# Optimization experiments

Hardware: AMD Instinct MI355X
Metric: run time of the kernel (lower is better)

Reference implementation:

```python
import jax, jax.numpy as jnp
import numpy as np

N_NODES = 100000
N_EDGES = 1600000
HID = 64
EPS = 1e-5


def setup_inputs() -> dict:
    key = jax.random.key(0)
    ks = jax.random.split(key, 16)
    d = {}
    d["x"] = jax.random.normal(ks[0], (N_NODES, 3), dtype=jnp.float32)
    d["edge_index"] = jax.random.randint(ks[1], (2, N_EDGES), 0, N_NODES, dtype=jnp.int64)
    # GCNConv weights (glorot-ish scaling)
    d["W1"] = jax.random.normal(ks[2], (3, HID), dtype=jnp.float32) * 0.3
    d["b1"] = jnp.zeros((HID,), jnp.float32)
    d["W2"] = jax.random.normal(ks[3], (HID, HID), dtype=jnp.float32) * (1.0 / np.sqrt(HID))
    d["b2"] = jnp.zeros((HID,), jnp.float32)
    d["W3"] = jax.random.normal(ks[4], (HID, HID), dtype=jnp.float32) * (1.0 / np.sqrt(HID))
    d["b3"] = jnp.zeros((HID,), jnp.float32)
    # edge predictor MLP: 128 -> 64 -> 32 -> 2 with BatchNorm after first two ReLUs
    d["Wm1"] = jax.random.normal(ks[5], (2 * HID, HID), dtype=jnp.float32) * (1.0 / np.sqrt(2 * HID))
    d["bm1"] = jnp.zeros((HID,), jnp.float32)
    d["g1"] = jnp.ones((HID,), jnp.float32)
    d["be1"] = jnp.zeros((HID,), jnp.float32)
    d["Wm2"] = jax.random.normal(ks[6], (HID, HID // 2), dtype=jnp.float32) * (1.0 / np.sqrt(HID))
    d["bm2"] = jnp.zeros((HID // 2,), jnp.float32)
    d["g2"] = jnp.ones((HID // 2,), jnp.float32)
    d["be2"] = jnp.zeros((HID // 2,), jnp.float32)
    d["Wm3"] = jax.random.normal(ks[7], (HID // 2, 2), dtype=jnp.float32) * (1.0 / np.sqrt(HID // 2))
    d["bm3"] = jnp.zeros((2,), jnp.float32)
    return d


def _gcn_conv(h_in, W, b, row, col, n_nodes):
    """PyG GCNConv: y = D^{-1/2}(A+I)D^{-1/2} (x W) + b (self-loops in row/col)."""
    h = h_in @ W  # [N, out]
    deg = jax.ops.segment_sum(jnp.ones_like(col, dtype=h.dtype), col, num_segments=n_nodes)
    dinv = jnp.where(deg > 0, jax.lax.rsqrt(deg), 0.0)
    norm = dinv[row] * dinv[col]  # [E+N]
    msg = h[row] * norm[:, None]  # gather + per-edge scale
    out = jax.ops.segment_sum(msg, col, num_segments=n_nodes)
    return out + b


def _batchnorm(x, gamma, beta):
    # training-mode batch statistics (biased variance), eps as in nn.BatchNorm1d
    mu = jnp.mean(x, axis=0)
    var = jnp.mean(jnp.square(x - mu), axis=0)
    return (x - mu) * jax.lax.rsqrt(var + EPS) * gamma + beta


def reference(x, edge_index, W1, b1, W2, b2, W3, b3,
              Wm1, bm1, g1, be1, Wm2, bm2, g2, be2, Wm3, bm3):
    n = x.shape[0]
    loops = jnp.arange(n, dtype=edge_index.dtype)
    row = jnp.concatenate([edge_index[0], loops])
    col = jnp.concatenate([edge_index[1], loops])

    h = jax.nn.relu(_gcn_conv(x, W1, b1, row, col, n))
    h = jax.nn.relu(_gcn_conv(h, W2, b2, row, col, n))
    h = _gcn_conv(h, W3, b3, row, col, n)

    src, dst = edge_index[0], edge_index[1]
    ef = jnp.concatenate([h[src], h[dst]], axis=1)  # [E, 2*HID]

    z = jax.nn.relu(ef @ Wm1 + bm1)
    z = _batchnorm(z, g1, be1)
    z = jax.nn.relu(z @ Wm2 + bm2)
    z = _batchnorm(z, g2, be2)
    return z @ Wm3 + bm3  # [E, 2]
```

## Files before the change

### kernel.cpp

```cpp
#include <hip/hip_runtime.h>
#include <hip/hip_bf16.h>
#include <cstdint>
#include <cstring>

#define NN 100000
#define NE 1600000
#define HID 64
#define EPS 1e-5f

typedef __bf16 bf16_t;
typedef __attribute__((ext_vector_type(8))) __bf16 bf16x8;
typedef __attribute__((ext_vector_type(4))) float f32x4;
typedef __attribute__((ext_vector_type(2))) float f32x2;
typedef __attribute__((ext_vector_type(16))) float f32x16;

#define LDS_FENCE() asm volatile("s_waitcnt lgkmcnt(0)" ::: "memory")

__global__ void k_detect(const unsigned* __restrict__ xw, const int* __restrict__ eiw,
                         int* __restrict__ flags) {
  int lane = threadIdx.x;
  unsigned u = xw[lane];
  unsigned lo = u & 0xFFFFu;
  unsigned e = (lo >> 7) & 0xFFu;
  bool bf_ok = (lo == 0u) || (e >= 0x50u && e <= 0x8Fu);
  unsigned long long b1 = __ballot(bf_ok);
  int v = eiw[2 * lane + 1];
  unsigned long long b2 = __ballot(v == 0);
  if (lane == 0) {
    flags[0] = (b1 == ~0ull) ? 1 : 0;
    flags[1] = (b2 == ~0ull) ? 1 : 0;
  }
}

struct FPtrs {
  const void* p[17];
  int len[17];
  int ofs[17];
};

template <typename FT>
__global__ void k_cvt_f(FPtrs fp, float* __restrict__ canon, const int* __restrict__ flags,
                        int total) {
  if (flags[0] != (int)(sizeof(FT) == 2)) return;
  int i = blockIdx.x * blockDim.x + threadIdx.x;
  int stride = gridDim.x * blockDim.x;
  for (int t = i; t < total; t += stride) {
    int seg = 0;
    while (seg < 16 && t >= fp.ofs[seg] + fp.len[seg]) ++seg;
    canon[t] = (float)((const FT*)fp.p[seg])[t - fp.ofs[seg]];
  }
}

template <typename IT>
__global__ void k_cvt_idx(const IT* __restrict__ ei, int* __restrict__ eic,
                          const int* __restrict__ flags) {
  if (flags[1] != (int)(sizeof(IT) == 8)) return;
  int i = blockIdx.x * blockDim.x + threadIdx.x;
  int stride = gridDim.x * blockDim.x;
  for (int t = i; t < 2 * NE; t += stride) eic[t] = (int)ei[t];
}

__global__ void k_zero4(f32x4* __restrict__ p, int n4) {
  int i = blockIdx.x * blockDim.x + threadIdx.x;
  int stride = gridDim.x * blockDim.x;
  f32x4 z = {0.f, 0.f, 0.f, 0.f};
  for (int t = i; t < n4; t += stride) p[t] = z;
}

__global__ void k_count(const int* __restrict__ col, int* __restrict__ cnt) {
  int i = blockIdx.x * blockDim.x + threadIdx.x;
  int stride = gridDim.x * blockDim.x;
  for (int e = i; e < NE; e += stride) atomicAdd(&cnt[col[e]], 1);
}

__global__ void k_dinv(const int* __restrict__ cnt, float* __restrict__ d) {
  int n = blockIdx.x * blockDim.x + threadIdx.x;
  if (n < NN) d[n] = rsqrtf((float)cnt[n] + 1.0f);
}

__global__ void k_scan1(const int* __restrict__ cnt, int* __restrict__ rowptr,
                        int* __restrict__ bsum, int nvals) {
  __shared__ int tmp[256];
  int gid = blockIdx.x * 256 + threadIdx.x;
  int v = (gid < nvals) ? cnt[gid] : 0;
  tmp[threadIdx.x] = v;
  __syncthreads();
  for (int s = 1; s < 256; s <<= 1) {
    int add = (threadIdx.x >= s) ? tmp[threadIdx.x - s] : 0;
    __syncthreads();
    tmp[threadIdx.x] += add;
    __syncthreads();
  }
  if (gid < nvals) rowptr[gid] = tmp[threadIdx.x] - v;
  if (threadIdx.x == 255) bsum[blockIdx.x] = tmp[255];
}

__global__ void k_scan2(int* __restrict__ bsum, int* __restrict__ btop, int nblocks) {
  __shared__ int tmp[512];
  int v = (threadIdx.x < nblocks) ? bsum[threadIdx.x] : 0;
  tmp[threadIdx.x] = v;
  __syncthreads();
  for (int s = 1; s < 512; s <<= 1) {
    int add = (threadIdx.x >= s) ? tmp[threadIdx.x - s] : 0;
    __syncthreads();
    tmp[threadIdx.x] += add;
    __syncthreads();
  }
  if (threadIdx.x < nblocks) btop[threadIdx.x] = tmp[threadIdx.x] - v;
}

__global__ void k_scan3(int* __restrict__ rowptr, const int* __restrict__ btop,
                        int* __restrict__ cursor, int nvals) {
  int gid = blockIdx.x * 256 + threadIdx.x;
  if (gid < nvals) {
    int v = rowptr[gid] + btop[blockIdx.x];
    rowptr[gid] = v;
    cursor[gid] = v;
  }
}

__global__ void k_fill(const int* __restrict__ eic, int* __restrict__ cursor,
                       int* __restrict__ csr_src) {
  int i = blockIdx.x * blockDim.x + threadIdx.x;
  int stride = gridDim.x * blockDim.x;
  for (int e = i; e < NE; e += stride) {
    int src = eic[e], dst = eic[NE + e];
    int pos = atomicAdd(&cursor[dst], 1);
    csr_src[pos] = src;
  }
}

__global__ void k_xs(const float* __restrict__ x, const float* __restrict__ dinv,
                     f32x4* __restrict__ xs4) {
  int n = blockIdx.x * blockDim.x + threadIdx.x;
  if (n >= NN) return;
  float d = dinv[n];
  f32x4 r = {x[n * 3 + 0] * d, x[n * 3 + 1] * d, x[n * 3 + 2] * d, 0.f};
  xs4[n] = r;
}

__global__ __launch_bounds__(256) void k_g1(const int* __restrict__ rowptr,
                                            const int* __restrict__ cnt,
                                            const int* __restrict__ csr_src,
                                            const f32x4* __restrict__ xs4,
                                            const float* __restrict__ dinv,
                                            f32x4* __restrict__ agg3) {
  int wid = (blockIdx.x * blockDim.x + threadIdx.x) >> 6;
  int nw = (gridDim.x * blockDim.x) >> 6;
  int lane = threadIdx.x & 63;
  int comp = lane & 3, slot = lane >> 2;
  for (int n = wid; n < NN; n += nw) {
    int beg = rowptr[n], c = cnt[n];
    float acc = 0.f;
    for (int k = slot; k < c; k += 16) {
      int src = csr_src[beg + k];
      acc += ((const float*)(xs4 + src))[comp];
    }
    acc += __shfl_xor(acc, 4); acc += __shfl_xor(acc, 8);
    acc += __shfl_xor(acc, 16); acc += __shfl_xor(acc, 32);
    if (lane < 4) {
      float self = ((const float*)(xs4 + n))[comp];
      ((float*)(agg3 + n))[comp] = (acc + self) * dinv[n];
    }
  }
}

__global__ __launch_bounds__(512) void k_f1(const f32x4* __restrict__ agg3,
                                            const float* __restrict__ W1f,
                                            const float* __restrict__ b1f,
                                            const float* __restrict__ W2f,
                                            const float* __restrict__ dinv,
                                            float* __restrict__ hs) {
  __shared__ float W1l[192];
  __shared__ float b1l[64];
  __shared__ float W2l[64 * 64];
  __shared__ float hrow[8][64];
  int tid = threadIdx.x;
  if (tid < 192) W1l[tid] = W1f[tid];
  if (tid < 64) b1l[tid] = b1f[tid];
  for (int i = tid; i < 64 * 64; i += 512) W2l[i] = W2f[i];
  __syncthreads();
  int w = tid >> 6, j = tid & 63;
  for (int nb = blockIdx.x * 8 + w; nb < NN; nb += gridDim.x * 8) {
    f32x4 a = agg3[nb];
    float h = fmaxf(a[0] * W1l[j] + a[1] * W1l[64 + j] + a[2] * W1l[128 + j] + b1l[j], 0.f);
    hrow[w][j] = h;
    LDS_FENCE();
    float acc = 0.f;
#pragma unroll 8
    for (int k = 0; k < 64; ++k) acc += hrow[w][k] * W2l[k * 64 + j];
    hs[nb * 64 + j] = acc * dinv[nb];
  }
}

__global__ __launch_bounds__(512) void k_g2(const int* __restrict__ rowptr,
                                            const int* __restrict__ cnt,
                                            const int* __restrict__ csr_src,
                                            const float* __restrict__ hs,
                                            const float* __restrict__ dinv,
                                            const float* __restrict__ b2f,
                                            const float* __restrict__ W3f,
                                            float* __restrict__ hs3) {
  __shared__ float W3l[64 * 64];
  __shared__ float hrow[8][64];
  int tid = threadIdx.x;
  for (int i = tid; i < 64 * 64; i += 512) W3l[i] = W3f[i];
  __syncthreads();
  int w = tid >> 6, j = tid & 63;
  float rb = b2f[j];
  for (int n = blockIdx.x * 8 + w; n < NN; n += gridDim.x * 8) {
    int beg = rowptr[n], c = cnt[n];
    float acc = hs[n * 64 + j];
    int k = 0;
    for (; k + 8 <= c; k += 8) {
      int s0 = csr_src[beg + k + 0], s1 = csr_src[beg + k + 1];
      int s2 = csr_src[beg + k + 2], s3 = csr_src[beg + k + 3];
      int s4 = csr_src[beg + k + 4], s5 = csr_src[beg + k + 5];
      int s6 = csr_src[beg + k + 6], s7 = csr_src[beg + k + 7];
      float v0 = hs[s0 * 64 + j], v1 = hs[s1 * 64 + j];
      float v2 = hs[s2 * 64 + j], v3 = hs[s3 * 64 + j];
      float v4 = hs[s4 * 64 + j], v5 = hs[s5 * 64 + j];
      float v6 = hs[s6 * 64 + j], v7 = hs[s7 * 64 + j];
      acc += ((v0 + v1) + (v2 + v3)) + ((v4 + v5) + (v6 + v7));
    }
    for (; k < c; ++k) acc += hs[csr_src[beg + k] * 64 + j];
    float h2 = fmaxf(acc * dinv[n] + rb, 0.f);
    hrow[w][j] = h2;
    LDS_FENCE();
    float s = 0.f;
#pragma unroll 8
    for (int kk = 0; kk < 64; ++kk) s += hrow[w][kk] * W3l[kk * 64 + j];
    hs3[n * 64 + j] = s * dinv[n];
  }
}

__global__ __launch_bounds__(512) void k_g3(const int* __restrict__ rowptr,
                                            const int* __restrict__ cnt,
                                            const int* __restrict__ csr_src,
                                            const float* __restrict__ hs3,
                                            const float* __restrict__ dinv,
                                            const float* __restrict__ b3f,
                                            const float* __restrict__ Wm1f,
                                            bf16_t* __restrict__ u, bf16_t* __restrict__ v) {
  __shared__ float Wt[64 * 64];
  __shared__ float Wb[64 * 64];
  __shared__ float hrow[8][64];
  int tid = threadIdx.x;
  for (int i = tid; i < 64 * 64; i += 512) {
    Wt[i] = Wm1f[i];
    Wb[i] = Wm1f[4096 + i];
  }
  __syncthreads();
  int w = tid >> 6, j = tid & 63;
  float rb = b3f[j];
  for (int n = blockIdx.x * 8 + w; n < NN; n += gridDim.x * 8) {
    int beg = rowptr[n], c = cnt[n];
    float acc = hs3[n * 64 + j];
    int k = 0;
    for (; k + 8 <= c; k += 8) {
      int s0 = csr_src[beg + k + 0], s1 = csr_src[beg + k + 1];
      int s2 = csr_src[beg + k + 2], s3 = csr_src[beg + k + 3];
      int s4 = csr_src[beg + k + 4], s5 = csr_src[beg + k + 5];
      int s6 = csr_src[beg + k + 6], s7 = csr_src[beg + k + 7];
      float v0 = hs3[s0 * 64 + j], v1 = hs3[s1 * 64 + j];
      float v2 = hs3[s2 * 64 + j], v3 = hs3[s3 * 64 + j];
      float v4 = hs3[s4 * 64 + j], v5 = hs3[s5 * 64 + j];
      float v6 = hs3[s6 * 64 + j], v7 = hs3[s7 * 64 + j];
      acc += ((v0 + v1) + (v2 + v3)) + ((v4 + v5) + (v6 + v7));
    }
    for (; k < c; ++k) acc += hs3[csr_src[beg + k] * 64 + j];
    float h3 = acc * dinv[n] + rb;
    hrow[w][j] = h3;
    LDS_FENCE();
    float au = 0.f, av = 0.f;
#pragma unroll 8
    for (int kk = 0; kk < 64; ++kk) {
      float hv = hrow[w][kk];
      au += hv * Wt[kk * 64 + j];
      av += hv * Wb[kk * 64 + j];
    }
    u[n * 64 + j] = (bf16_t)au;
    v[n * 64 + j] = (bf16_t)av;
  }
}

__global__ __launch_bounds__(256) void k_e1(const int* __restrict__ eic,
                                            const bf16_t* __restrict__ u,
                                            const bf16_t* __restrict__ v,
                                            const float* __restrict__ bm1f,
                                            float* __restrict__ sum1,
                                            float* __restrict__ sq1) {
  __shared__ float reds[16][16];
  __shared__ float redq[16][16];
  int lane = threadIdx.x & 63;
  int wv = threadIdx.x >> 6;
  int wave = blockIdx.x * 4 + wv;
  int nwaves = gridDim.x * 4;
  int n = lane & 15, q = lane >> 4;
  f32x16 bk;
#pragma unroll
  for (int j = 0; j < 8; ++j) {
    bk[j] = bm1f[q * 8 + j];
    bk[8 + j] = bm1f[32 + q * 8 + j];
  }
  f32x16 accs = {};
  f32x16 accq = {};
#pragma unroll 2
  for (int t = wave; t < NE / 16; t += nwaves) {
    int e = t * 16 + n;
    int src = eic[e], dst = eic[NE + e];
    const bf16x8* pu = (const bf16x8*)(u + src * 64);
    const bf16x8* pv = (const bf16x8*)(v + dst * 64);
    bf16x8 ua = pu[q], ub = pu[4 + q], va = pv[q], vb = pv[4 + q];
    f32x16 a1k;
#pragma unroll
    for (int j = 0; j < 8; ++j) {
      a1k[j] = fmaxf((float)ua[j] + (float)va[j] + bk[j], 0.f);
      a1k[8 + j] = fmaxf((float)ub[j] + (float)vb[j] + bk[8 + j], 0.f);
    }
    accs += a1k;
    accq += a1k * a1k;
  }
#pragma unroll
  for (int j = 0; j < 16; ++j) {
    float s = accs[j], qq = accq[j];
    s += __shfl_xor(s, 1); s += __shfl_xor(s, 2);
    s += __shfl_xor(s, 4); s += __shfl_xor(s, 8);
    qq += __shfl_xor(qq, 1); qq += __shfl_xor(qq, 2);
    qq += __shfl_xor(qq, 4); qq += __shfl_xor(qq, 8);
    if (n == 0) {
      reds[wv * 4 + q][j] = s;
      redq[wv * 4 + q][j] = qq;
    }
  }
  __syncthreads();
  int tid = threadIdx.x;
  if (tid < 64) {
    int jq = (tid & 31) >> 3, elem = (tid >> 5) * 8 + (tid & 7);
    float s = reds[jq][elem] + reds[4 + jq][elem] + reds[8 + jq][elem] + reds[12 + jq][elem];
    float qq = redq[jq][elem] + redq[4 + jq][elem] + redq[8 + jq][elem] + redq[12 + jq][elem];
    unsafeAtomicAdd(&sum1[tid], s);
    unsafeAtomicAdd(&sq1[tid], qq);
  }
}

__global__ void k_bnconst(const float* __restrict__ sum, const float* __restrict__ sq,
                          const float* __restrict__ g, const float* __restrict__ be,
                          float* __restrict__ sarr, float* __restrict__ tarr, int ncol) {
  int j = threadIdx.x;
  if (j >= ncol) return;
  float mu = sum[j] / (float)NE;
  float var = fmaxf(sq[j] / (float)NE - mu * mu, 0.f);
  float s = g[j] * rsqrtf(var + EPS);
  sarr[j] = s;
  tarr[j] = be[j] - mu * s;
}

template <bool STORE>
__global__ __launch_bounds__(256) void k_e2(const int* __restrict__ eic,
                                            const bf16_t* __restrict__ u,
                                            const bf16_t* __restrict__ v,
                                            const float* __restrict__ bm1f,
                                            const float* __restrict__ s1, const float* __restrict__ t1,
                                            const float* __restrict__ Wm2f,
                                            const float* __restrict__ bm2f,
                                            bf16_t* __restrict__ a2s,
                                            float* __restrict__ sum2,
                                            float* __restrict__ sq2) {
  __shared__ float red2[4][4][16];
  int lane = threadIdx.x & 63;
  int wv = threadIdx.x >> 6;
  int wave = blockIdx.x * 4 + wv;
  int nwaves = gridDim.x * 4;
  int n = lane & 15, q = lane >> 4;
  f32x16 bk, s1k, t1k;
#pragma unroll
  for (int j = 0; j < 8; ++j) {
    bk[j] = bm1f[q * 8 + j];       bk[8 + j] = bm1f[32 + q * 8 + j];
    s1k[j] = s1[q * 8 + j];        s1k[8 + j] = s1[32 + q * 8 + j];
    t1k[j] = t1[q * 8 + j];        t1k[8 + j] = t1[32 + q * 8 + j];
  }
  bf16x8 b2h00, b2h01, b2h10, b2h11;
#pragma unroll
  for (int j = 0; j < 8; ++j) {
    b2h00[j] = (bf16_t)Wm2f[(q * 8 + j) * 32 + 0 * 16 + n];
    b2h01[j] = (bf16_t)Wm2f[(q * 8 + j) * 32 + 1 * 16 + n];
    b2h10[j] = (bf16_t)Wm2f[(32 + q * 8 + j) * 32 + 0 * 16 + n];
    b2h11[j] = (bf16_t)Wm2f[(32 + q * 8 + j) * 32 + 1 * 16 + n];
  }
  float bias20 = bm2f[n], bias21 = bm2f[16 + n];
  float accs0 = 0.f, accs1 = 0.f, accq0 = 0.f, accq1 = 0.f;
  for (int t = wave; t < NE / 16; t += nwaves) {
    int e = t * 16 + n;
    int src = eic[e], dst = eic[NE + e];
    const bf16x8* pu = (const bf16x8*)(u + src * 64);
    const bf16x8* pv = (const bf16x8*)(v + dst * 64);
    bf16x8 ua = pu[q], ub = pu[4 + q], va = pv[q], vb = pv[4 + q];
    f32x16 a1k;
#pragma unroll
    for (int j = 0; j < 8; ++j) {
      a1k[j] = fmaxf((float)ua[j] + (float)va[j] + bk[j], 0.f);
      a1k[8 + j] = fmaxf((float)ub[j] + (float)vb[j] + bk[8 + j], 0.f);
    }
    f32x16 z = a1k * s1k + t1k;
    bf16x8 g0h, g0l, g1h, g1l;
#pragma unroll
    for (int j = 0; j < 8; ++j) {
      float z0 = z[j], z1 = z[8 + j];
      bf16_t h0 = (bf16_t)z0, h1 = (bf16_t)z1;
      g0h[j] = h0; g0l[j] = (bf16_t)(z0 - (float)h0);
      g1h[j] = h1; g1l[j] = (bf16_t)(z1 - (float)h1);
    }
    f32x4 c0 = {0.f, 0.f, 0.f, 0.f}, c1 = {0.f, 0.f, 0.f, 0.f};
    c0 = __builtin_amdgcn_mfma_f32_16x16x32_bf16(g0h, b2h00, c0, 0, 0, 0);
    c0 = __builtin_amdgcn_mfma_f32_16x16x32_bf16(g0l, b2h00, c0, 0, 0, 0);
    c0 = __builtin_amdgcn_mfma_f32_16x16x32_bf16(g1h, b2h10, c0, 0, 0, 0);
    c0 = __builtin_amdgcn_mfma_f32_16x16x32_bf16(g1l, b2h10, c0, 0, 0, 0);
    c1 = __builtin_amdgcn_mfma_f32_16x16x32_bf16(g0h, b2h01, c1, 0, 0, 0);
    c1 = __builtin_amdgcn_mfma_f32_16x16x32_bf16(g0l, b2h01, c1, 0, 0, 0);
    c1 = __builtin_amdgcn_mfma_f32_16x16x32_bf16(g1h, b2h11, c1, 0, 0, 0);
    c1 = __builtin_amdgcn_mfma_f32_16x16x32_bf16(g1l, b2h11, c1, 0, 0, 0);
#pragma unroll
    for (int r = 0; r < 4; ++r) {
      float v0 = fmaxf(c0[r] + bias20, 0.f);
      float v1 = fmaxf(c1[r] + bias21, 0.f);
      if (STORE) {
        a2s[(size_t)(t * 16 + q * 4 + r) * 32 + n] = (bf16_t)v0;
        a2s[(size_t)(t * 16 + q * 4 + r) * 32 + 16 + n] = (bf16_t)v1;
      }
      accs0 += v0; accq0 += v0 * v0;
      accs1 += v1; accq1 += v1 * v1;
    }
  }
  accs0 += __shfl_xor(accs0, 16); accs0 += __shfl_xor(accs0, 32);
  accq0 += __shfl_xor(accq0, 16); accq0 += __shfl_xor(accq0, 32);
  accs1 += __shfl_xor(accs1, 16); accs1 += __shfl_xor(accs1, 32);
  accq1 += __shfl_xor(accq1, 16); accq1 += __shfl_xor(accq1, 32);
  if (lane < 16) {
    red2[wv][0][lane] = accs0;
    red2[wv][1][lane] = accq0;
    red2[wv][2][lane] = accs1;
    red2[wv][3][lane] = accq1;
  }
  __syncthreads();
  int tid = threadIdx.x;
  if (tid < 32) {
    int which = tid >> 4, nn = tid & 15;
    float s = red2[0][which * 2][nn] + red2[1][which * 2][nn] + red2[2][which * 2][nn] +
              red2[3][which * 2][nn];
    float qq = red2[0][which * 2 + 1][nn] + red2[1][which * 2 + 1][nn] +
               red2[2][which * 2 + 1][nn] + red2[3][which * 2 + 1][nn];
    unsafeAtomicAdd(&sum2[tid], s);
    unsafeAtomicAdd(&sq2[tid], qq);
  }
}

template <typename OT>
__global__ __launch_bounds__(256) void k_out_stream(const bf16_t* __restrict__ a2s,
                                                    const float* __restrict__ s2,
                                                    const float* __restrict__ t2,
                                                    const float* __restrict__ Wm3f,
                                                    const float* __restrict__ bm3f,
                                                    OT* __restrict__ out,
                                                    const int* __restrict__ flags) {
  if (flags[0] != (int)(sizeof(OT) == 2)) return;
  int lane = threadIdx.x & 63;
  int wave = blockIdx.x * 4 + (threadIdx.x >> 6);
  int nwaves = gridDim.x * 4;
  int half = lane & 1;
  int sub = lane >> 1;
  f32x16 s2c, t2c, w0, w1;
#pragma unroll
  for (int i = 0; i < 16; ++i) {
    int c = half * 16 + i;
    s2c[i] = s2[c]; t2c[i] = t2[c];
    w0[i] = Wm3f[c * 2 + 0]; w1[i] = Wm3f[c * 2 + 1];
  }
  float bb0 = bm3f[0], bb1 = bm3f[1];
  const int ntiles = NE / 32;
#pragma unroll 2
  for (int t = wave; t < ntiles; t += nwaves) {
    int e = t * 32 + sub;
    const bf16x8* pa = (const bf16x8*)(a2s + (size_t)e * 32 + half * 16);
    bf16x8 v0 = pa[0], v1 = pa[1];
    float o0 = 0.f, o1 = 0.f;
#pragma unroll
    for (int i = 0; i < 8; ++i) {
      float z = (float)v0[i] * s2c[i] + t2c[i];
      o0 += z * w0[i]; o1 += z * w1[i];
      float z2 = (float)v1[i] * s2c[8 + i] + t2c[8 + i];
      o0 += z2 * w0[8 + i]; o1 += z2 * w1[8 + i];
    }
    o0 += __shfl_xor(o0, 1);
    o1 += __shfl_xor(o1, 1);
    if (half == 0) {
      o0 += bb0; o1 += bb1;
      if (sizeof(OT) == 2) {
        bf16_t p[2] = {(bf16_t)o0, (bf16_t)o1};
        unsigned pw;
        memcpy(&pw, p, 4);
        ((unsigned*)out)[e] = pw;
      } else {
        f32x2 pw = {o0, o1};
        ((f32x2*)out)[e] = pw;
      }
    }
  }
}

template <typename OT>
__global__ __launch_bounds__(256) void k_out_recomp(const int* __restrict__ eic,
                                                    const bf16_t* __restrict__ u,
                                                    const bf16_t* __restrict__ v,
                                                    const float* __restrict__ bm1f,
                                                    const float* __restrict__ s1, const float* __restrict__ t1,
                                                    const float* __restrict__ Wm2f,
                                                    const float* __restrict__ bm2f,
                                                    const float* __restrict__ s2, const float* __restrict__ t2,
                                                    const float* __restrict__ Wm3f,
                                                    const float* __restrict__ bm3f,
                                                    OT* __restrict__ out,
                                                    const int* __restrict__ flags) {
  if (flags[0] != (int)(sizeof(OT) == 2)) return;
  int lane = threadIdx.x & 63;
  int wave = blockIdx.x * 4 + (threadIdx.x >> 6);
  int nwaves = gridDim.x * 4;
  int n = lane & 15, q = lane >> 4;
  f32x16 bk, s1k, t1k;
#pragma unroll
  for (int j = 0; j < 8; ++j) {
    bk[j] = bm1f[q * 8 + j];       bk[8 + j] = bm1f[32 + q * 8 + j];
    s1k[j] = s1[q * 8 + j];        s1k[8 + j] = s1[32 + q * 8 + j];
    t1k[j] = t1[q * 8 + j];        t1k[8 + j] = t1[32 + q * 8 + j];
  }
  bf16x8 b2h00, b2h01, b2h10, b2h11;
#pragma unroll
  for (int j = 0; j < 8; ++j) {
    b2h00[j] = (bf16_t)Wm2f[(q * 8 + j) * 32 + 0 * 16 + n];
    b2h01[j] = (bf16_t)Wm2f[(q * 8 + j) * 32 + 1 * 16 + n];
    b2h10[j] = (bf16_t)Wm2f[(32 + q * 8 + j) * 32 + 0 * 16 + n];
    b2h11[j] = (bf16_t)Wm2f[(32 + q * 8 + j) * 32 + 1 * 16 + n];
  }
  float bias20 = bm2f[n], bias21 = bm2f[16 + n];
  float s2c0 = s2[n], t2c0 = t2[n], s2c1 = s2[16 + n], t2c1 = t2[16 + n];
  float w3a0 = Wm3f[n * 2 + 0], w3a1 = Wm3f[n * 2 + 1];
  float w3b0 = Wm3f[(16 + n) * 2 + 0], w3b1 = Wm3f[(16 + n) * 2 + 1];
  float bb0 = bm3f[0], bb1 = bm3f[1];

  for (int t = wave; t < NE / 16; t += nwaves) {
    int e = t * 16 + n;
    int src = eic[e], dst = eic[NE + e];
    const bf16x8* pu = (const bf16x8*)(u + src * 64);
    const bf16x8* pv = (const bf16x8*)(v + dst * 64);
    bf16x8 ua = pu[q], ub = pu[4 + q], va = pv[q], vb = pv[4 + q];
    f32x16 a1k;
#pragma unroll
    for (int j = 0; j < 8; ++j) {
      a1k[j] = fmaxf((float)ua[j] + (float)va[j] + bk[j], 0.f);
      a1k[8 + j] = fmaxf((float)ub[j] + (float)vb[j] + bk[8 + j], 0.f);
    }
    f32x16 z = a1k * s1k + t1k;
    bf16x8 g0h, g0l, g1h, g1l;
#pragma unroll
    for (int j = 0; j < 8; ++j) {
      float z0 = z[j], z1 = z[8 + j];
      bf16_t h0 = (bf16_t)z0, h1 = (bf16_t)z1;
      g0h[j] = h0; g0l[j] = (bf16_t)(z0 - (float)h0);
      g1h[j] = h1; g1l[j] = (bf16_t)(z1 - (float)h1);
    }
    f32x4 c0 = {0.f, 0.f, 0.f, 0.f}, c1 = {0.f, 0.f, 0.f, 0.f};
    c0 = __builtin_amdgcn_mfma_f32_16x16x32_bf16(g0h, b2h00, c0, 0, 0, 0);
    c0 = __builtin_amdgcn_mfma_f32_16x16x32_bf16(g0l, b2h00, c0, 0, 0, 0);
    c0 = __builtin_amdgcn_mfma_f32_16x16x32_bf16(g1h, b2h10, c0, 0, 0, 0);
    c0 = __builtin_amdgcn_mfma_f32_16x16x32_bf16(g1l, b2h10, c0, 0, 0, 0);
    c1 = __builtin_amdgcn_mfma_f32_16x16x32_bf16(g0h, b2h01, c1, 0, 0, 0);
    c1 = __builtin_amdgcn_mfma_f32_16x16x32_bf16(g0l, b2h01, c1, 0, 0, 0);
    c1 = __builtin_amdgcn_mfma_f32_16x16x32_bf16(g1h, b2h11, c1, 0, 0, 0);
    c1 = __builtin_amdgcn_mfma_f32_16x16x32_bf16(g1l, b2h11, c1, 0, 0, 0);
#pragma unroll
    for (int r = 0; r < 4; ++r) {
      float z0 = fmaxf(c0[r] + bias20, 0.f) * s2c0 + t2c0;
      float z1 = fmaxf(c1[r] + bias21, 0.f) * s2c1 + t2c1;
      float o0 = z0 * w3a0 + z1 * w3b0;
      float o1 = z0 * w3a1 + z1 * w3b1;
      o0 += __shfl_xor(o0, 1); o0 += __shfl_xor(o0, 2);
      o0 += __shfl_xor(o0, 4); o0 += __shfl_xor(o0, 8);
      o1 += __shfl_xor(o1, 1); o1 += __shfl_xor(o1, 2);
      o1 += __shfl_xor(o1, 4); o1 += __shfl_xor(o1, 8);
      if (n == 0) {
        int eo = t * 16 + q * 4 + r;
        o0 += bb0; o1 += bb1;
        if (sizeof(OT) == 2) {
          bf16_t p[2] = {(bf16_t)o0, (bf16_t)o1};
          unsigned pw;
          memcpy(&pw, p, 4);
          ((unsigned*)out)[eo] = pw;
        } else {
          f32x2 pw = {o0, o1};
          ((f32x2*)out)[eo] = pw;
        }
      }
    }
  }
}

extern "C" void kernel_launch(void* const* d_in, const int* in_sizes, int n_in,
                              void* d_out, int out_size, void* d_ws, size_t ws_size,
                              hipStream_t stream) {
  (void)n_in; (void)in_sizes; (void)out_size;

  char* ws = (char*)d_ws;
  size_t off = 0;
  auto alloc = [&](size_t bytes) {
    size_t r = off;
    off = (off + bytes + 255) & ~(size_t)255;
    return r;
  };
  float* dinv  = (float*)(ws + alloc((size_t)NN * 4));
  float* hs    = (float*)(ws + alloc((size_t)NN * HID * 4));
  float* agg   = (float*)(ws + alloc((size_t)NN * HID * 4));
  int*   eic   = (int*)(ws + alloc((size_t)2 * NE * 4));
  float* stats = (float*)(ws + alloc(192 * 4));
  float* sum1 = stats, *sq1 = stats + 64, *sum2 = stats + 128, *sq2 = stats + 160;
  int*   flags = (int*)(ws + alloc(256));
  float* s1arr = (float*)(ws + alloc(64 * 4));
  float* t1arr = (float*)(ws + alloc(64 * 4));
  float* s2arr = (float*)(ws + alloc(32 * 4));
  float* t2arr = (float*)(ws + alloc(32 * 4));
  int* cnt     = (int*)(ws + alloc((size_t)NN * 4));
  int* rowptr  = (int*)(ws + alloc((size_t)NN * 4));
  int* cursor  = (int*)(ws + alloc((size_t)NN * 4));
  int* bsum    = (int*)(ws + alloc(512 * 4));
  int* btop    = (int*)(ws + alloc(512 * 4));
  int* csr_src = (int*)(ws + alloc((size_t)NE * 4));
  bf16_t* u    = (bf16_t*)(ws + alloc((size_t)NN * HID * 2));
  bf16_t* v    = (bf16_t*)(ws + alloc((size_t)NN * HID * 2));
  f32x4* xs4   = (f32x4*)(ws + alloc((size_t)NN * 16));
  f32x4* agg3  = (f32x4*)(ws + alloc((size_t)NN * 16));

  static const int flens[17] = {NN * 3, 3 * 64, 64, 64 * 64, 64, 64 * 64, 64,
                                128 * 64, 64, 64, 64, 64 * 32, 32, 32, 32, 32 * 2, 2};
  FPtrs fp;
  int total_f = 0;
  {
    int fi = 0;
    for (int i = 0; i < 18; ++i) {
      if (i == 1) continue;
      fp.p[fi] = d_in[i];
      fp.len[fi] = flens[fi];
      fp.ofs[fi] = total_f;
      total_f += flens[fi];
      ++fi;
    }
  }
  float* canon = (float*)(ws + alloc((size_t)total_f * 4));
  size_t a2_off = alloc((size_t)NE * 32 * 2);
  bf16_t* a2s = (bf16_t*)(ws + a2_off);
  bool tierB = (a2_off + (size_t)NE * 32 * 2) <= ws_size;

  const float* xf   = canon + fp.ofs[0];
  const float* W1f  = canon + fp.ofs[1];
  const float* b1f  = canon + fp.ofs[2];
  const float* W2f  = canon + fp.ofs[3];
  const float* b2f  = canon + fp.ofs[4];
  const float* W3f  = canon + fp.ofs[5];
  const float* b3f  = canon + fp.ofs[6];
  const float* Wm1f = canon + fp.ofs[7];
  const float* bm1f = canon + fp.ofs[8];
  const float* g1f  = canon + fp.ofs[9];
  const float* be1f = canon + fp.ofs[10];
  const float* Wm2f = canon + fp.ofs[11];
  const float* bm2f = canon + fp.ofs[12];
  const float* g2f  = canon + fp.ofs[13];
  const float* be2f = canon + fp.ofs[14];
  const float* Wm3f = canon + fp.ofs[15];
  const float* bm3f = canon + fp.ofs[16];

  const int nscanb = (NN + 255) / 256;

  k_detect<<<1, 64, 0, stream>>>((const unsigned*)d_in[0], (const int*)d_in[1], flags);
  k_cvt_idx<int><<<1600, 256, 0, stream>>>((const int*)d_in[1], eic, flags);
  k_cvt_idx<long long><<<1600, 256, 0, stream>>>((const long long*)d_in[1], eic, flags);
  k_cvt_f<float><<<640, 256, 0, stream>>>(fp, canon, flags, total_f);
  k_cvt_f<bf16_t><<<640, 256, 0, stream>>>(fp, canon, flags, total_f);

  k_zero4<<<128, 256, 0, stream>>>((f32x4*)cnt, NN / 4);
  k_zero4<<<1, 64, 0, stream>>>((f32x4*)stats, 48);
  k_count<<<1600, 256, 0, stream>>>(eic + NE, cnt);
  k_dinv<<<(NN + 255) / 256, 256, 0, stream>>>(cnt, dinv);
  k_scan1<<<nscanb, 256, 0, stream>>>(cnt, rowptr, bsum, NN);
  k_scan2<<<1, 512, 0, stream>>>(bsum, btop, nscanb);
  k_scan3<<<nscanb, 256, 0, stream>>>(rowptr, btop, cursor, NN);
  k_fill<<<1600, 256, 0, stream>>>(eic, cursor, csr_src);

  k_xs<<<(NN + 255) / 256, 256, 0, stream>>>(xf, dinv, xs4);
  k_g1<<<2048, 256, 0, stream>>>(rowptr, cnt, csr_src, xs4, dinv, agg3);
  k_f1<<<1024, 512, 0, stream>>>(agg3, W1f, b1f, W2f, dinv, hs);

  k_g2<<<1024, 512, 0, stream>>>(rowptr, cnt, csr_src, hs, dinv, b2f, W3f, agg);

  k_g3<<<1024, 512, 0, stream>>>(rowptr, cnt, csr_src, agg, dinv, b3f, Wm1f, u, v);

  k_e1<<<2048, 256, 0, stream>>>(eic, u, v, bm1f, sum1, sq1);
  k_bnconst<<<1, 64, 0, stream>>>(sum1, sq1, g1f, be1f, s1arr, t1arr, 64);
  if (tierB) {
    k_e2<true><<<2048, 256, 0, stream>>>(eic, u, v, bm1f, s1arr, t1arr, Wm2f, bm2f, a2s,
                                         sum2, sq2);
    k_bnconst<<<1, 64, 0, stream>>>(sum2, sq2, g2f, be2f, s2arr, t2arr, 32);
    k_out_stream<float><<<2048, 256, 0, stream>>>(a2s, s2arr, t2arr, Wm3f, bm3f,
                                                  (float*)d_out, flags);
    k_out_stream<bf16_t><<<2048, 256, 0, stream>>>(a2s, s2arr, t2arr, Wm3f, bm3f,
                                                   (bf16_t*)d_out, flags);
  } else {
    k_e2<false><<<2048, 256, 0, stream>>>(eic, u, v, bm1f, s1arr, t1arr, Wm2f, bm2f, a2s,
                                          sum2, sq2);
    k_bnconst<<<1, 64, 0, stream>>>(sum2, sq2, g2f, be2f, s2arr, t2arr, 32);
    k_out_recomp<float><<<2048, 256, 0, stream>>>(eic, u, v, bm1f, s1arr, t1arr, Wm2f,
                                                  bm2f, s2arr, t2arr, Wm3f, bm3f,
                                                  (float*)d_out, flags);
    k_out_recomp<bf16_t><<<2048, 256, 0, stream>>>(eic, u, v, bm1f, s1arr, t1arr, Wm2f,
                                                   bm2f, s2arr, t2arr, Wm3f, bm3f,
                                                   (bf16_t*)d_out, flags);
  }
}
```

Measured before the change: 780.6 us.

## Build CSR via two-pass bucketed partition instead of global atomic scatter

Replaces the global-atomic CSR fill with a two-pass radix-style partition. Edges are first bucketed by destination range (128 buckets of 782 nodes) into a staging buffer using block-local histograms. A second pass then scatters each bucket into csr_src using LDS cursors. The aim is to cut contended global atomics and the random scattered writes, at the cost of an extra 12.8MB staging write and read and more kernel launches. The bucket-count pass now runs in only 200 blocks.

```diff
diff --git a/kernel.cpp b/kernel.cpp
--- a/kernel.cpp
+++ b/kernel.cpp
@@ -7,6 +7,8 @@
 #define NE 1600000
 #define HID 64
 #define EPS 1e-5f
+#define NB1 128
+#define BSZ 782
 
 typedef __bf16 bf16_t;
 typedef __attribute__((ext_vector_type(8))) __bf16 bf16x8;
@@ -67,10 +69,21 @@
   for (int t = i; t < n4; t += stride) p[t] = z;
 }
 
-__global__ void k_count(const int* __restrict__ col, int* __restrict__ cnt) {
-  int i = blockIdx.x * blockDim.x + threadIdx.x;
-  int stride = gridDim.x * blockDim.x;
-  for (int e = i; e < NE; e += stride) atomicAdd(&cnt[col[e]], 1);
+__global__ __launch_bounds__(256) void k_cnt2(const int* __restrict__ dstp,
+                                              int* __restrict__ cnt, int* __restrict__ bcnt) {
+  __shared__ int lh[NB1];
+  int tid = threadIdx.x;
+  if (tid < NB1) lh[tid] = 0;
+  __syncthreads();
+  const int per = NE / 200;
+  int e0 = blockIdx.x * per;
+  for (int k = tid; k < per; k += 256) {
+    int dst = dstp[e0 + k];
+    atomicAdd(&cnt[dst], 1);
+    atomicAdd(&lh[dst / BSZ], 1);
+  }
+  __syncthreads();
+  if (tid < NB1) atomicAdd(&bcnt[tid], lh[tid]);
 }
 
 __global__ void k_dinv(const int* __restrict__ cnt, float* __restrict__ d) {
@@ -109,23 +122,101 @@
   if (threadIdx.x < nblocks) btop[threadIdx.x] = tmp[threadIdx.x] - v;
 }
 
-__global__ void k_scan3(int* __restrict__ rowptr, const int* __restrict__ btop,
-                        int* __restrict__ cursor, int nvals) {
+__global__ void k_scan3(int* __restrict__ rowptr, const int* __restrict__ btop, int nvals) {
   int gid = blockIdx.x * 256 + threadIdx.x;
-  if (gid < nvals) {
-    int v = rowptr[gid] + btop[blockIdx.x];
-    rowptr[gid] = v;
-    cursor[gid] = v;
-  }
-}
-
-__global__ void k_fill(const int* __restrict__ eic, int* __restrict__ cursor,
-                       int* __restrict__ csr_src) {
-  int i = blockIdx.x * blockDim.x + threadIdx.x;
-  int stride = gridDim.x * blockDim.x;
-  for (int e = i; e < NE; e += stride) {
-    int src = eic[e], dst = eic[NE + e];
-    int pos = atomicAdd(&cursor[dst], 1);
+  if (gid < nvals) rowptr[gid] += btop[blockIdx.x];
+}
+
+__global__ void k_scanb(const int* __restrict__ bcnt, int* __restrict__ bptr,
+                        int* __restrict__ bcur) {
+  __shared__ int tmp[NB1];
+  int j = threadIdx.x;
+  int v = bcnt[j];
+  tmp[j] = v;
+  __syncthreads();
+  for (int s = 1; s < NB1; s <<= 1) {
+    int a = (j >= s) ? tmp[j - s] : 0;
+    __syncthreads();
+    tmp[j] += a;
+    __syncthreads();
+  }
+  bptr[j] = tmp[j] - v;
+  bcur[j] = tmp[j] - v;
+}
+
+__global__ __launch_bounds__(256) void k_p1(const int* __restrict__ eic,
+                                            int* __restrict__ bcur,
+                                            long long* __restrict__ staging) {
+  __shared__ long long buf[2048];
+  __shared__ int tgt[2048];
+  __shared__ int hist[NB1], lbase[NB1], gbase[NB1];
+  int tid = threadIdx.x;
+  int e0 = blockIdx.x * 2048;
+  int cntE = NE - e0;
+  if (cntE > 2048) cntE = 2048;
+  if (tid < NB1) hist[tid] = 0;
+  __syncthreads();
+  int slotk[8], bk[8];
+  long long pk[8];
+#pragma unroll
+  for (int k = 0; k < 8; ++k) {
+    int i = k * 256 + tid;
+    bk[k] = -1;
+    if (i < cntE) {
+      int e = e0 + i;
+      int src = eic[e], dst = eic[NE + e];
+      bk[k] = dst / BSZ;
+      pk[k] = ((long long)(unsigned)src) | (((long long)(unsigned)dst) << 32);
+      slotk[k] = atomicAdd(&hist[bk[k]], 1);
+    }
+  }
+  __syncthreads();
+  if (tid < NB1) lbase[tid] = hist[tid];
+  __syncthreads();
+  for (int s = 1; s < NB1; s <<= 1) {
+    int a = 0;
+    if (tid < NB1 && tid >= s) a = lbase[tid - s];
+    __syncthreads();
+    if (tid < NB1) lbase[tid] += a;
+    __syncthreads();
+  }
+  if (tid < NB1) {
+    int exc = lbase[tid] - hist[tid];
+    lbase[tid] = exc;
+    gbase[tid] = (hist[tid] > 0) ? atomicAdd(&bcur[tid], hist[tid]) : 0;
+  }
+  __syncthreads();
+#pragma unroll
+  for (int k = 0; k < 8; ++k) {
+    if (bk[k] >= 0) {
+      int idx = lbase[bk[k]] + slotk[k];
+      buf[idx] = pk[k];
+      tgt[idx] = gbase[bk[k]] + slotk[k];
+    }
+  }
+  __syncthreads();
+  for (int i = tid; i < cntE; i += 256) staging[tgt[i]] = buf[i];
+}
+
+__global__ __launch_bounds__(256) void k_p2(const long long* __restrict__ staging,
+                                            const int* __restrict__ bptr,
+                                            const int* __restrict__ bcnt,
+                                            const int* __restrict__ rowptr,
+                                            int* __restrict__ csr_src) {
+  __shared__ int lcur[BSZ];
+  int b = blockIdx.x;
+  int nb0 = b * BSZ;
+  int nN = NN - nb0;
+  if (nN > BSZ) nN = BSZ;
+  int tid = threadIdx.x;
+  for (int i = tid; i < nN; i += 256) lcur[i] = rowptr[nb0 + i];
+  __syncthreads();
+  int beg = bptr[b], cntE = bcnt[b];
+  for (int k = tid; k < cntE; k += 256) {
+    long long p = staging[beg + k];
+    int src = (int)(p & 0xffffffffLL);
+    int dst = (int)(p >> 32);
+    int pos = atomicAdd(&lcur[dst - nb0], 1);
     csr_src[pos] = src;
   }
 }
@@ -629,10 +720,13 @@
   float* t2arr = (float*)(ws + alloc(32 * 4));
   int* cnt     = (int*)(ws + alloc((size_t)NN * 4));
   int* rowptr  = (int*)(ws + alloc((size_t)NN * 4));
-  int* cursor  = (int*)(ws + alloc((size_t)NN * 4));
   int* bsum    = (int*)(ws + alloc(512 * 4));
   int* btop    = (int*)(ws + alloc(512 * 4));
+  int* bcnt    = (int*)(ws + alloc(NB1 * 4));
+  int* bptr    = (int*)(ws + alloc(NB1 * 4));
+  int* bcur    = (int*)(ws + alloc(NB1 * 4));
   int* csr_src = (int*)(ws + alloc((size_t)NE * 4));
+  long long* staging = (long long*)(ws + alloc((size_t)NE * 8));
   bf16_t* u    = (bf16_t*)(ws + alloc((size_t)NN * HID * 2));
   bf16_t* v    = (bf16_t*)(ws + alloc((size_t)NN * HID * 2));
   f32x4* xs4   = (f32x4*)(ws + alloc((size_t)NN * 16));
@@ -686,12 +780,15 @@
 
   k_zero4<<<128, 256, 0, stream>>>((f32x4*)cnt, NN / 4);
   k_zero4<<<1, 64, 0, stream>>>((f32x4*)stats, 48);
-  k_count<<<1600, 256, 0, stream>>>(eic + NE, cnt);
+  k_zero4<<<1, 32, 0, stream>>>((f32x4*)bcnt, NB1 / 4);
+  k_cnt2<<<200, 256, 0, stream>>>(eic + NE, cnt, bcnt);
   k_dinv<<<(NN + 255) / 256, 256, 0, stream>>>(cnt, dinv);
   k_scan1<<<nscanb, 256, 0, stream>>>(cnt, rowptr, bsum, NN);
   k_scan2<<<1, 512, 0, stream>>>(bsum, btop, nscanb);
-  k_scan3<<<nscanb, 256, 0, stream>>>(rowptr, btop, cursor, NN);
-  k_fill<<<1600, 256, 0, stream>>>(eic, cursor, csr_src);
+  k_scan3<<<nscanb, 256, 0, stream>>>(rowptr, btop, NN);
+  k_scanb<<<1, NB1, 0, stream>>>(bcnt, bptr, bcur);
+  k_p1<<<(NE + 2047) / 2048, 256, 0, stream>>>(eic, bcur, staging);
+  k_p2<<<NB1, 256, 0, stream>>>(staging, bptr, bcnt, rowptr, csr_src);
 
   k_xs<<<(NN + 255) / 256, 256, 0, stream>>>(xf, dinv, xs4);
   k_g1<<<2048, 256, 0, stream>>>(rowptr, cnt, csr_src, xs4, dinv, agg3);
```

New measurement: 699.5 us. 1.12x faster.
